# Kernel tuning notes

Hardware: AMD Instinct MI355X
Metric: run time of the kernel (lower is better)

## Reference

```python
import jax, jax.numpy as jnp
import numpy as np

S, B, W, D2 = 128, 64, 32, 512   # sen_len, batch, wiki_len, 2*eh_size
DH = 512                          # dh_size


def setup_inputs() -> dict:
    key = jax.random.key(0)
    ks = jax.random.split(key, 8)
    inp = {
        "i": 0,
        "valid_sen": jnp.arange(B, dtype=jnp.int64) if jax.config.jax_enable_x64 else jnp.arange(B, dtype=jnp.int32),
        "reverse_valid_sen": jnp.arange(B, dtype=jnp.int32),
        "wiki_sen": jax.random.randint(ks[0], (B, W, S), 0, 32000),
        "wiki_num": jax.random.randint(ks[1], (B,), 0, W),
        "h1": jax.random.normal(ks[2], (S, B, W, D2), dtype=jnp.float32),
        "h_n1": jax.random.normal(ks[3], (W, B, D2), dtype=jnp.float32),
        "atten_label": jax.random.randint(ks[4], (B,), 0, W),
        "h": jax.random.normal(ks[5], (B, D2), dtype=jnp.float32),
        "h_n": jax.random.normal(ks[6], (B, D2), dtype=jnp.float32),
        # initLinearLayer: Linear(4*eh -> dh)
        "W_init": jax.random.normal(ks[7], (DH, 2 * D2), dtype=jnp.float32) / np.sqrt(2 * D2),
        "b_init": jnp.zeros((DH,), dtype=jnp.float32),
    }
    inp["valid_sen"] = jnp.arange(B, dtype=jnp.int32)
    return inp


def reference(i, valid_sen, reverse_valid_sen, wiki_sen, wiki_num, h1, h_n1,
              atten_label, h, h_n, W_init, b_init):
    # --- gather valid sentences (index_select) ---
    vw_hn1 = h_n1[:, valid_sen]        # [W, Bv, D2]
    v_wiki_sen = wiki_sen[valid_sen]   # [Bv, W, S]
    v_h1 = h1[:, valid_sen]            # [S, Bv, W, D2]
    lbl = atten_label[valid_sen]       # [Bv]

    # --- attention scores: beta[b, w] = <h_n1[w, b], h_n[b]> ---
    beta = jnp.einsum('wbd,bd->bw', vw_hn1, h_n)  # [Bv, W]

    # --- CrossEntropyLoss(ignore_index=0) ---
    logp = jax.nn.log_softmax(beta, axis=1)
    nll = -jnp.take_along_axis(logp, lbl[:, None], axis=1)[:, 0]   # [Bv]
    valid = (lbl != 0)
    cnt = valid.sum().astype(beta.dtype)
    atten_loss = jnp.where(cnt > 0,
                           jnp.sum(jnp.where(valid, nll, 0.0)) / jnp.maximum(cnt, 1.0),
                           0.0)

    # --- golden (scatter one-hot) hard alignment -> context vector ---
    Bv = beta.shape[0]
    b_idx = jnp.arange(Bv)
    wiki_cv = vw_hn1[lbl, b_idx]                   # [Bv, D2]  (== sum over one-hot)

    # --- init hidden for decoder ---
    init_h = jnp.concatenate([h_n, wiki_cv], axis=1) @ W_init.T + b_init  # [Bv, DH]

    # --- select aligned wiki sentence / hidden states ---
    selected_wiki_h = v_h1[:, b_idx, lbl].transpose(1, 0, 2)  # [Bv, S, D2]
    selected_wiki_sen = v_wiki_sen[b_idx, lbl]                # [Bv, S]

    return (selected_wiki_sen, selected_wiki_h, init_h, wiki_cv, atten_loss)
```

## Files before the change

kernel.cpp:

```cpp
#include <hip/hip_runtime.h>

#define S 128
#define B 64
#define W 32
#define D2 512
#define DH 512

#define OFF_SEN 0
#define OFF_SWH (B * S)
#define OFF_INITH (OFF_SWH + B * S * D2)
#define OFF_CV (OFF_INITH + B * DH)
#define OFF_LOSS (OFF_CV + B * D2)

#define NB_BETA 64
#define NB_INITH 128
#define NB_GATHER 1024
#define NB_TOTAL (NB_BETA + NB_INITH + NB_GATHER)

__global__ __launch_bounds__(256) void k_fused(
    const float* __restrict__ h1, const float* __restrict__ h_n1,
    const float* __restrict__ h_n, const float* __restrict__ Wi,
    const float* __restrict__ bi, const int* __restrict__ wiki_sen,
    const int* __restrict__ valid_sen, const int* __restrict__ atten_label,
    float* __restrict__ out, float* __restrict__ ws)
{
    __shared__ float smem[4 * 2 * D2];
    const int bid = blockIdx.x;
    const int tid = threadIdx.x;

    if (bid < NB_BETA) {
        const int b = bid;
        const int lane = tid & 63;
        const int wv = tid >> 6;
        const int vs = valid_sen[b];
        const int lbl = atten_label[vs];
        float* sbeta = smem;

        const float* hb = h_n + b * D2;
        const float4 hn0 = ((const float4*)hb)[lane];
        const float4 hn1 = ((const float4*)hb)[64 + lane];

        #pragma unroll
        for (int i = 0; i < 8; ++i) {
            const int w = wv * 8 + i;
            const float* row = h_n1 + (w * B + vs) * D2;
            const float4 a0 = ((const float4*)row)[lane];
            const float4 a1 = ((const float4*)row)[64 + lane];
            float p = a0.x * hn0.x + a0.y * hn0.y + a0.z * hn0.z + a0.w * hn0.w
                    + a1.x * hn1.x + a1.y * hn1.y + a1.z * hn1.z + a1.w * hn1.w;
            #pragma unroll
            for (int m = 32; m >= 1; m >>= 1) p += __shfl_xor(p, m);
            if (lane == 0) sbeta[w] = p;
        }
        __syncthreads();

        if (tid == 0) {
            float mx = sbeta[0];
            for (int w = 1; w < W; ++w) mx = fmaxf(mx, sbeta[w]);
            float Z = 0.0f;
            for (int w = 0; w < W; ++w) Z += expf(sbeta[w] - mx);
            const float nll = -(sbeta[lbl] - mx - logf(Z));
            ws[b] = nll;
            ws[B + b] = (lbl != 0) ? 1.0f : 0.0f;
        }

        if (tid < 128) {
            const float4* src = (const float4*)(h_n1 + (lbl * B + vs) * D2);
            float4* dst = (float4*)(out + OFF_CV + b * D2);
            dst[tid] = src[tid];
        }
    } else if (bid < NB_BETA + NB_INITH) {
        float (*wrow)[2 * D2] = (float (*)[2 * D2])smem;
        const int kt = (bid - NB_BETA) * 4;

        #pragma unroll
        for (int kk = 0; kk < 4; ++kk) {
            ((float4*)wrow[kk])[tid] =
                ((const float4*)(Wi + (size_t)(kt + kk) * (2 * D2)))[tid];
        }
        __syncthreads();

        const int b = tid >> 2;
        const int kk = tid & 3;
        const int k = kt + kk;
        const int vs = valid_sen[b];
        const int lbl = atten_label[vs];
        float acc = bi[k];
        const float4* hb = (const float4*)(h_n + b * D2);
        const float4* cb = (const float4*)(h_n1 + (lbl * B + vs) * D2);
        const float4* w0 = (const float4*)wrow[kk];
        const float4* w1 = (const float4*)(wrow[kk] + D2);
        #pragma unroll 4
        for (int d = 0; d < D2 / 4; ++d) {
            const float4 a = hb[d], w = w0[d];
            acc += a.x * w.x + a.y * w.y + a.z * w.z + a.w * w.w;
        }
        #pragma unroll 4
        for (int d = 0; d < D2 / 4; ++d) {
            const float4 a = cb[d], w = w1[d];
            acc += a.x * w.x + a.y * w.y + a.z * w.z + a.w * w.w;
        }
        out[OFF_INITH + b * DH + k] = acc;
    } else {
        const int Q = B * S * (D2 / 4);
        const int gid = (bid - NB_BETA - NB_INITH) * 256 + tid;

        if (gid < B * S) {
            const int b = gid >> 7, s = gid & 127;
            const int vs = valid_sen[b];
            const int lbl = atten_label[vs];
            out[OFF_SEN + gid] = (float)wiki_sen[(vs * W + lbl) * S + s];
        }

        const int stride = NB_GATHER * 256;
        for (int q = gid; q < Q; q += stride) {
            const int d4 = q & 127;
            const int t = q >> 7;
            const int s = t & 127;
            const int b = t >> 7;
            const int vs = valid_sen[b];
            const int lbl = atten_label[vs];
            const float4* src = (const float4*)(h1 + ((size_t)((s * B + vs) * W + lbl) * D2));
            ((float4*)(out + OFF_SWH))[q] = src[d4];
        }
    }
}

__global__ void k_loss(const float* __restrict__ ws, float* __restrict__ out)
{
    const int t = threadIdx.x;
    float nll = ws[t];
    float v = ws[B + t];
    float sn = v * nll;
    float sc = v;
    #pragma unroll
    for (int m = 32; m >= 1; m >>= 1) {
        sn += __shfl_xor(sn, m);
        sc += __shfl_xor(sc, m);
    }
    if (t == 0) out[OFF_LOSS] = (sc > 0.0f) ? sn / fmaxf(sc, 1.0f) : 0.0f;
}

extern "C" void kernel_launch(void* const* d_in, const int* in_sizes, int n_in,
                              void* d_out, int out_size, void* d_ws, size_t ws_size,
                              hipStream_t stream) {
    const int* valid_sen   = (const int*)d_in[1];
    const int* wiki_sen    = (const int*)d_in[3];
    const float* h1        = (const float*)d_in[5];
    const float* h_n1      = (const float*)d_in[6];
    const int* atten_label = (const int*)d_in[7];
    const float* h_n       = (const float*)d_in[9];
    const float* Wi        = (const float*)d_in[10];
    const float* bi        = (const float*)d_in[11];
    float* out = (float*)d_out;
    float* ws  = (float*)d_ws;

    k_fused<<<NB_TOTAL, 256, 0, stream>>>(h1, h_n1, h_n, Wi, bi, wiki_sen,
                                          valid_sen, atten_label, out, ws);
    k_loss<<<1, 64, 0, stream>>>(ws, out);
}
```

Measured before the change: 26.02 us.

## Fold loss reduction into fused kernel via last-block atomic counter, widen gather grid

Removes the separate loss kernel launch. The last of the 64 beta blocks to finish, found through an atomic counter in workspace, now computes the loss. A memset on the counter is added before the launch. The gather section doubles its block count to a fixed two iterations per thread and caches each batch's row index (valid_sen*W+label) in shared memory, avoiding repeated dependent index loads. The context-vector copy is moved before the barrier so it overlaps the beta reduction. The memset adds its own stream operation, which may offset part of the saving from dropping the loss kernel.

```diff
diff --git a/kernel.cpp b/kernel.cpp
--- a/kernel.cpp
+++ b/kernel.cpp
@@ -12,9 +12,11 @@
 #define OFF_CV (OFF_INITH + B * DH)
 #define OFF_LOSS (OFF_CV + B * D2)
 
+#define WS_CNT_BYTE_OFF 512
+
 #define NB_BETA 64
 #define NB_INITH 128
-#define NB_GATHER 1024
+#define NB_GATHER 2048
 #define NB_TOTAL (NB_BETA + NB_INITH + NB_GATHER)
 
 __global__ __launch_bounds__(256) void k_fused(
@@ -52,6 +54,12 @@
             for (int m = 32; m >= 1; m >>= 1) p += __shfl_xor(p, m);
             if (lane == 0) sbeta[w] = p;
         }
+
+        if (tid < 128) {
+            const float4* src = (const float4*)(h_n1 + (lbl * B + vs) * D2);
+            float4* dst = (float4*)(out + OFF_CV + b * D2);
+            dst[tid] = src[tid];
+        }
         __syncthreads();
 
         if (tid == 0) {
@@ -60,14 +68,22 @@
             float Z = 0.0f;
             for (int w = 0; w < W; ++w) Z += expf(sbeta[w] - mx);
             const float nll = -(sbeta[lbl] - mx - logf(Z));
-            ws[b] = nll;
-            ws[B + b] = (lbl != 0) ? 1.0f : 0.0f;
-        }
-
-        if (tid < 128) {
-            const float4* src = (const float4*)(h_n1 + (lbl * B + vs) * D2);
-            float4* dst = (float4*)(out + OFF_CV + b * D2);
-            dst[tid] = src[tid];
+            atomicExch(&ws[b], nll);
+            atomicExch(&ws[B + b], (lbl != 0) ? 1.0f : 0.0f);
+            __threadfence();
+            unsigned* cnt = (unsigned*)((char*)ws + WS_CNT_BYTE_OFF);
+            const unsigned old = atomicAdd(cnt, 1u);
+            if (old == NB_BETA - 1) {
+                __threadfence();
+                float sn = 0.0f, sc = 0.0f;
+                for (int i = 0; i < B; ++i) {
+                    const float nv = atomicAdd(&ws[i], 0.0f);
+                    const float vv = atomicAdd(&ws[B + i], 0.0f);
+                    sn += vv * nv;
+                    sc += vv;
+                }
+                out[OFF_LOSS] = (sc > 0.0f) ? sn / fmaxf(sc, 1.0f) : 0.0f;
+            }
         }
     } else if (bid < NB_BETA + NB_INITH) {
         float (*wrow)[2 * D2] = (float (*)[2 * D2])smem;
@@ -102,43 +118,31 @@
         }
         out[OFF_INITH + b * DH + k] = acc;
     } else {
-        const int Q = B * S * (D2 / 4);
+        int* gi = (int*)smem;
+        if (tid < B) {
+            const int vs = valid_sen[tid];
+            gi[tid] = vs * W + atten_label[vs];
+        }
+        __syncthreads();
+
         const int gid = (bid - NB_BETA - NB_INITH) * 256 + tid;
 
         if (gid < B * S) {
             const int b = gid >> 7, s = gid & 127;
-            const int vs = valid_sen[b];
-            const int lbl = atten_label[vs];
-            out[OFF_SEN + gid] = (float)wiki_sen[(vs * W + lbl) * S + s];
+            out[OFF_SEN + gid] = (float)wiki_sen[gi[b] * S + s];
         }
 
-        const int stride = NB_GATHER * 256;
-        for (int q = gid; q < Q; q += stride) {
+        #pragma unroll
+        for (int it = 0; it < 2; ++it) {
+            const int q = gid + it * (NB_GATHER * 256);
             const int d4 = q & 127;
             const int t = q >> 7;
             const int s = t & 127;
             const int b = t >> 7;
-            const int vs = valid_sen[b];
-            const int lbl = atten_label[vs];
-            const float4* src = (const float4*)(h1 + ((size_t)((s * B + vs) * W + lbl) * D2));
+            const float4* src = (const float4*)(h1 + ((size_t)(s * (B * W) + gi[b])) * D2);
             ((float4*)(out + OFF_SWH))[q] = src[d4];
         }
     }
-}
-
-__global__ void k_loss(const float* __restrict__ ws, float* __restrict__ out)
-{
-    const int t = threadIdx.x;
-    float nll = ws[t];
-    float v = ws[B + t];
-    float sn = v * nll;
-    float sc = v;
-    #pragma unroll
-    for (int m = 32; m >= 1; m >>= 1) {
-        sn += __shfl_xor(sn, m);
-        sc += __shfl_xor(sc, m);
-    }
-    if (t == 0) out[OFF_LOSS] = (sc > 0.0f) ? sn / fmaxf(sc, 1.0f) : 0.0f;
 }
 
 extern "C" void kernel_launch(void* const* d_in, const int* in_sizes, int n_in,
@@ -155,7 +159,8 @@
     float* out = (float*)d_out;
     float* ws  = (float*)d_ws;
 
+    hipMemsetAsync((char*)d_ws + WS_CNT_BYTE_OFF, 0, 4, stream);
+
     k_fused<<<NB_TOTAL, 256, 0, stream>>>(h1, h_n1, h_n, Wi, bi, wiki_sen,
                                           valid_sen, atten_label, out, ws);
-    k_loss<<<1, 64, 0, stream>>>(ws, out);
 }
```

Result: slower. 59.49 us (+128.7%).
